# Kernel tuning notes

Hardware: AMD Instinct MI355X
Metric: run time of the kernel (lower is better)

The kernel has to match this reference:

```python
import jax, jax.numpy as jnp
import numpy as np

B, S, UNITS = 64, 2048, 1024


def setup_inputs() -> dict:
    key = jax.random.key(0)
    ks = jax.random.split(key, 6)
    scale = 1.0 / np.sqrt(UNITS)
    return {
        "s_prev": jax.random.normal(ks[0], (B, UNITS), dtype=jnp.float32),
        "hidden_states": jax.random.normal(ks[1], (B, S, UNITS), dtype=jnp.float32),
        "W_w": jax.random.normal(ks[2], (UNITS, UNITS), dtype=jnp.float32) * scale,
        "W_b": jnp.zeros((UNITS,), dtype=jnp.float32),
        "U_w": jax.random.normal(ks[3], (UNITS, UNITS), dtype=jnp.float32) * scale,
        "U_b": jnp.zeros((UNITS,), dtype=jnp.float32),
        "V_w": jax.random.normal(ks[4], (UNITS, 1), dtype=jnp.float32) * scale,
        "V_b": jnp.zeros((1,), dtype=jnp.float32),
    }


def reference(s_prev, hidden_states, W_w, W_b, U_w, U_b, V_w, V_b):
    # W(s_prev): [B, units] -> [B, 1, units]
    W_s = (s_prev @ W_w + W_b)[:, None, :]
    # U(hidden_states): [B, S, units]
    U_h = jnp.einsum('bsu,uk->bsk', hidden_states, U_w) + U_b
    # V(tanh(W_s + U_h)): [B, S, 1]
    scores = jnp.tanh(W_s + U_h) @ V_w + V_b
    # softmax over seq axis
    weights = jax.nn.softmax(scores, axis=1)  # [B, S, 1]
    # weighted sum over seq -> context [B, units]
    context = jnp.sum(weights * hidden_states, axis=1)
    return context, weights
```

## Files before the change

### kernel.cpp

```cpp
#include <hip/hip_runtime.h>

#define BB   64
#define SS   2048
#define UU   1024
#define MM   (BB * SS)

typedef unsigned short u16;
typedef unsigned int   u32;
typedef __attribute__((ext_vector_type(8))) short bf16x8;
typedef __attribute__((ext_vector_type(4))) float f32x4;

__device__ __forceinline__ u16 f2b(float f) {
    u32 x = __float_as_uint(f);
    u32 r = (x + 0x7fffu + ((x >> 16) & 1u)) >> 16;
    return (u16)r;
}
__device__ __forceinline__ float b2f(u16 u) {
    return __uint_as_float(((u32)u) << 16);
}
__device__ __forceinline__ float fast_tanh(float x) {
    x = fminf(fmaxf(x, -15.f), 15.f);
    float e = __expf(2.f * x);
    return (e - 1.f) / (e + 1.f);
}
__device__ __forceinline__ void async_copy16(const u16* gp, u16* lp) {
    __builtin_amdgcn_global_load_lds(
        (const __attribute__((address_space(1))) unsigned int*)gp,
        (__attribute__((address_space(3))) unsigned int*)lp, 16, 0, 0);
}

#define WAITV(N) asm volatile("s_waitcnt vmcnt(" #N ")" ::: "memory")

__global__ __launch_bounds__(256) void k_transpose_uw(const float* __restrict__ Uw,
                                                      u16* __restrict__ UwT) {
    __shared__ float tile[64][65];
    int n0 = blockIdx.x * 64, k0 = blockIdx.y * 64;
    int c = threadIdx.x & 63, r0 = threadIdx.x >> 6;
#pragma unroll
    for (int i = 0; i < 64; i += 4)
        tile[r0 + i][c] = Uw[(size_t)(k0 + r0 + i) * UU + n0 + c];
    __syncthreads();
#pragma unroll
    for (int i = 0; i < 64; i += 4)
        UwT[(size_t)(n0 + r0 + i) * UU + k0 + c] = f2b(tile[c][r0 + i]);
}

__global__ __launch_bounds__(256) void k_convert_h(const float* __restrict__ src,
                                                   u16* __restrict__ dst) {
    size_t i = ((size_t)blockIdx.x * 256 + threadIdx.x) * 8;
    float4 f0 = *(const float4*)(src + i);
    float4 f1 = *(const float4*)(src + i + 4);
    u16 t[8];
    t[0] = f2b(f0.x); t[1] = f2b(f0.y); t[2] = f2b(f0.z); t[3] = f2b(f0.w);
    t[4] = f2b(f1.x); t[5] = f2b(f1.y); t[6] = f2b(f1.z); t[7] = f2b(f1.w);
    *(uint4*)(dst + i) = *(uint4*)t;
}

__global__ __launch_bounds__(256) void k_ws(const float* __restrict__ sp,
                                            const float* __restrict__ Ww,
                                            const float* __restrict__ Wb,
                                            float* __restrict__ Ws) {
    int u = blockIdx.x * 256 + threadIdx.x;
    int b = blockIdx.y;
    int k0 = blockIdx.z * 256;
    const float* sprow = sp + (size_t)b * UU + k0;
    float acc = (blockIdx.z == 0) ? Wb[u] : 0.f;
#pragma unroll 4
    for (int k = 0; k < 256; ++k)
        acc = fmaf(sprow[k], Ww[(size_t)(k0 + k) * UU + u], acc);
    atomicAdd(&Ws[(size_t)b * UU + u], acc);
}

__global__ __launch_bounds__(512, 2) void k_gemm256(const u16* __restrict__ A,
                                                    const u16* __restrict__ UwT,
                                                    const float* __restrict__ Ws,
                                                    const float* __restrict__ Ub,
                                                    const float* __restrict__ Vw,
                                                    float* __restrict__ scp) {
    __shared__ __align__(16) u16 As[4][8192];
    __shared__ __align__(16) u16 Bs[4][8192];
    const int tid  = threadIdx.x;
    const int lane = tid & 63;
    const int wave = tid >> 6;
    const int wm = wave >> 2;
    const int wn = wave & 3;
    const int quad = lane >> 4, l15 = lane & 15;

    const int bid = blockIdx.x;
    const int xcd = bid & 7;
    const int li  = bid >> 3;
    const int mt  = xcd * 64 + (li >> 2);
    const int nt  = li & 3;
    const size_t m0 = (size_t)mt * 256;
    const int n0  = nt * 256;

    const int srow   = lane >> 2;
    const int schunk = (lane & 3) ^ ((srow >> 1) & 3);
    const size_t lane_off = (size_t)srow * UU + (size_t)schunk * 8;
    const int gA = wave * 2;

    int offA[8], offB[4];
#pragma unroll
    for (int mi = 0; mi < 8; ++mi) {
        int r = wm * 128 + mi * 16 + l15;
        offA[mi] = r * 32 + (quad ^ ((r >> 1) & 3)) * 8;
    }
#pragma unroll
    for (int ni = 0; ni < 4; ++ni) {
        int r = wn * 64 + ni * 16 + l15;
        offB[ni] = r * 32 + (quad ^ ((r >> 1) & 3)) * 8;
    }

    f32x4 acc[8][4];
#pragma unroll
    for (int i = 0; i < 8; ++i)
#pragma unroll
        for (int j = 0; j < 4; ++j) acc[i][j] = (f32x4){0.f, 0.f, 0.f, 0.f};

    const u16* Abase = A + m0 * UU;
    const u16* Bbase = UwT + (size_t)n0 * UU;

#define STAGE(kt) do {                                                         \
        const int _b = (kt) & 3;                                               \
        const u16* _ga = Abase + (size_t)(gA * 16) * UU + (kt) * 32 + lane_off;\
        async_copy16(_ga,                  &As[_b][gA * 512]);                 \
        async_copy16(_ga + (size_t)16 * UU, &As[_b][(gA + 1) * 512]);          \
        const u16* _gb = Bbase + (size_t)(gA * 16) * UU + (kt) * 32 + lane_off;\
        async_copy16(_gb,                  &Bs[_b][gA * 512]);                 \
        async_copy16(_gb + (size_t)16 * UU, &Bs[_b][(gA + 1) * 512]);          \
    } while (0)

    auto compute = [&](int kt) {
        const u16* ab = As[kt & 3];
        const u16* bb = Bs[kt & 3];
        bf16x8 a[8], b[4];
#pragma unroll
        for (int mi = 0; mi < 8; ++mi) a[mi] = *(const bf16x8*)(ab + offA[mi]);
#pragma unroll
        for (int ni = 0; ni < 4; ++ni) b[ni] = *(const bf16x8*)(bb + offB[ni]);
        __builtin_amdgcn_s_setprio(1);
#pragma unroll
        for (int mi = 0; mi < 8; ++mi)
#pragma unroll
            for (int ni = 0; ni < 4; ++ni)
                acc[mi][ni] = __builtin_amdgcn_mfma_f32_16x16x32_bf16(
                    a[mi], b[ni], acc[mi][ni], 0, 0, 0);
        __builtin_amdgcn_s_setprio(0);
    };

    STAGE(0); STAGE(1); STAGE(2);

    for (int kt = 0; kt < 29; ++kt) {
        WAITV(8);
        __builtin_amdgcn_sched_barrier(0);
        __builtin_amdgcn_s_barrier();
        STAGE(kt + 3);
        compute(kt);
    }
    WAITV(8); __builtin_amdgcn_sched_barrier(0); __builtin_amdgcn_s_barrier(); compute(29);
    WAITV(4); __builtin_amdgcn_sched_barrier(0); __builtin_amdgcn_s_barrier(); compute(30);
    WAITV(0); __builtin_amdgcn_sched_barrier(0); __builtin_amdgcn_s_barrier(); compute(31);
#undef STAGE

    const int bidx = (int)(m0 >> 11);
    const float* wsrow = Ws + (size_t)bidx * UU;
    float wsv[4], ubv[4], vwv[4];
#pragma unroll
    for (int ni = 0; ni < 4; ++ni) {
        int ng = n0 + wn * 64 + ni * 16 + l15;
        wsv[ni] = wsrow[ng];
        ubv[ni] = Ub[ng];
        vwv[ni] = Vw[ng];
    }
#pragma unroll
    for (int mi = 0; mi < 8; ++mi) {
#pragma unroll
        for (int r = 0; r < 4; ++r) {
            float v = 0.f;
#pragma unroll
            for (int ni = 0; ni < 4; ++ni) {
                float x = acc[mi][ni][r] + wsv[ni] + ubv[ni];
                v = fmaf(fast_tanh(x), vwv[ni], v);
            }
#pragma unroll
            for (int off = 1; off < 16; off <<= 1)
                v += __shfl_xor(v, off, 64);
            if (l15 == 0) {
                size_t mg = m0 + wm * 128 + mi * 16 + quad * 4 + r;
                scp[mg * 16 + nt * 4 + wn] = v;
            }
        }
    }
}

__global__ __launch_bounds__(256) void k_gemm_f32(const float* __restrict__ Aptr,
                                                  const u16* __restrict__ UwT,
                                                  const float* __restrict__ Ws,
                                                  const float* __restrict__ Ub,
                                                  const float* __restrict__ Vw,
                                                  float* __restrict__ scp) {
    __shared__ __align__(16) u16 As[128][72];
    __shared__ __align__(16) u16 Bs[128][72];
    const int tid  = threadIdx.x;
    const int lane = tid & 63;
    const int wave = tid >> 6;
    const int wm = wave >> 1, wn = wave & 1;
    const int quad = lane >> 4, l15 = lane & 15;
    const int nt = blockIdx.x;
    const int n0 = nt * 128;
    const size_t m0 = (size_t)blockIdx.y * 128;

    f32x4 acc[4][4];
#pragma unroll
    for (int i = 0; i < 4; ++i)
#pragma unroll
        for (int j = 0; j < 4; ++j) acc[i][j] = (f32x4){0.f, 0.f, 0.f, 0.f};

    const int sr = tid >> 3;
    const int sc = (tid & 7) * 8;

    for (int kk = 0; kk < UU; kk += 64) {
#pragma unroll
        for (int i = 0; i < 4; ++i) {
            int r = sr + i * 32;
            const float4* p = (const float4*)(Aptr + (m0 + r) * UU + kk + sc);
            float4 f0 = p[0], f1 = p[1];
            u16 t[8];
            t[0] = f2b(f0.x); t[1] = f2b(f0.y); t[2] = f2b(f0.z); t[3] = f2b(f0.w);
            t[4] = f2b(f1.x); t[5] = f2b(f1.y); t[6] = f2b(f1.z); t[7] = f2b(f1.w);
            *(uint4*)(&As[r][sc]) = *(uint4*)t;
        }
#pragma unroll
        for (int i = 0; i < 4; ++i) {
            int r = sr + i * 32;
            uint4 v = *(const uint4*)(UwT + (size_t)(n0 + r) * UU + kk + sc);
            *(uint4*)(&Bs[r][sc]) = v;
        }
        __syncthreads();
#pragma unroll
        for (int k2 = 0; k2 < 64; k2 += 32) {
            bf16x8 a[4], b[4];
#pragma unroll
            for (int mi = 0; mi < 4; ++mi)
                a[mi] = *(const bf16x8*)(&As[wm * 64 + mi * 16 + l15][k2 + quad * 8]);
#pragma unroll
            for (int ni = 0; ni < 4; ++ni)
                b[ni] = *(const bf16x8*)(&Bs[wn * 64 + ni * 16 + l15][k2 + quad * 8]);
#pragma unroll
            for (int mi = 0; mi < 4; ++mi)
#pragma unroll
                for (int ni = 0; ni < 4; ++ni)
                    acc[mi][ni] = __builtin_amdgcn_mfma_f32_16x16x32_bf16(
                        a[mi], b[ni], acc[mi][ni], 0, 0, 0);
        }
        __syncthreads();
    }

    const int bidx = (int)(m0 >> 11);
    const float* wsrow = Ws + (size_t)bidx * UU;
    float wsv[4], ubv[4], vwv[4];
#pragma unroll
    for (int ni = 0; ni < 4; ++ni) {
        int ng = n0 + wn * 64 + ni * 16 + l15;
        wsv[ni] = wsrow[ng];
        ubv[ni] = Ub[ng];
        vwv[ni] = Vw[ng];
    }
#pragma unroll
    for (int mi = 0; mi < 4; ++mi) {
#pragma unroll
        for (int r = 0; r < 4; ++r) {
            float v = 0.f;
#pragma unroll
            for (int ni = 0; ni < 4; ++ni) {
                float x = acc[mi][ni][r] + wsv[ni] + ubv[ni];
                v = fmaf(fast_tanh(x), vwv[ni], v);
            }
#pragma unroll
            for (int off = 1; off < 16; off <<= 1)
                v += __shfl_xor(v, off, 64);
            if (l15 == 0) {
                size_t mg = m0 + wm * 64 + mi * 16 + quad * 4 + r;
                scp[mg * 16 + nt * 2 + wn] = v;
            }
        }
    }
}

__global__ __launch_bounds__(256) void k_softmax(const float* __restrict__ scp,
                                                 float* __restrict__ wout) {
    int b = blockIdx.x, t = threadIdx.x;
    __shared__ float red[256];
    float sc[8];
    float lmax = -1e30f;
#pragma unroll
    for (int i = 0; i < 8; ++i) {
        int s = t + i * 256;
        const float4* p = (const float4*)(scp + ((size_t)b * SS + s) * 16);
        float4 a = p[0], c = p[1], d = p[2], e = p[3];
        float v = (a.x + a.y + a.z + a.w) + (c.x + c.y + c.z + c.w) +
                  (d.x + d.y + d.z + d.w) + (e.x + e.y + e.z + e.w);
        sc[i] = v;
        lmax = fmaxf(lmax, v);
    }
    red[t] = lmax;
    __syncthreads();
    for (int o = 128; o > 0; o >>= 1) {
        if (t < o) red[t] = fmaxf(red[t], red[t + o]);
        __syncthreads();
    }
    float mx = red[0];
    __syncthreads();
    float lsum = 0.f;
#pragma unroll
    for (int i = 0; i < 8; ++i) {
        sc[i] = __expf(sc[i] - mx);
        lsum += sc[i];
    }
    red[t] = lsum;
    __syncthreads();
    for (int o = 128; o > 0; o >>= 1) {
        if (t < o) red[t] += red[t + o];
        __syncthreads();
    }
    float inv = 1.f / red[0];
#pragma unroll
    for (int i = 0; i < 8; ++i)
        wout[(size_t)b * SS + t + i * 256] = sc[i] * inv;
}

template <bool HBF16>
__global__ __launch_bounds__(256) void k_context(const void* __restrict__ hptr,
                                                 const float* __restrict__ w,
                                                 float* __restrict__ ctx) {
    int b = blockIdx.y;
    int s0 = blockIdx.x * 128;
    int u = threadIdx.x * 4;
    const float* wrow = w + (size_t)b * SS + s0;
    float a0 = 0.f, a1 = 0.f, a2 = 0.f, a3 = 0.f;
    for (int i = 0; i < 128; ++i) {
        float wv = wrow[i];
        size_t base = ((size_t)b * SS + s0 + i) * UU + u;
        if (HBF16) {
            ushort4 hv = *(const ushort4*)((const u16*)hptr + base);
            a0 = fmaf(wv, b2f(hv.x), a0);
            a1 = fmaf(wv, b2f(hv.y), a1);
            a2 = fmaf(wv, b2f(hv.z), a2);
            a3 = fmaf(wv, b2f(hv.w), a3);
        } else {
            float4 hv = *(const float4*)((const float*)hptr + base);
            a0 = fmaf(wv, hv.x, a0);
            a1 = fmaf(wv, hv.y, a1);
            a2 = fmaf(wv, hv.z, a2);
            a3 = fmaf(wv, hv.w, a3);
        }
    }
    atomicAdd(&ctx[(size_t)b * UU + u + 0], a0);
    atomicAdd(&ctx[(size_t)b * UU + u + 1], a1);
    atomicAdd(&ctx[(size_t)b * UU + u + 2], a2);
    atomicAdd(&ctx[(size_t)b * UU + u + 3], a3);
}

extern "C" void kernel_launch(void* const* d_in, const int* in_sizes, int n_in,
                              void* d_out, int out_size, void* d_ws, size_t ws_size,
                              hipStream_t stream) {
    const float* s_prev = (const float*)d_in[0];
    const float* h      = (const float*)d_in[1];
    const float* Ww     = (const float*)d_in[2];
    const float* Wb     = (const float*)d_in[3];
    const float* Uw     = (const float*)d_in[4];
    const float* Ub     = (const float*)d_in[5];
    const float* Vw     = (const float*)d_in[6];

    float* out = (float*)d_out;
    char* ws = (char*)d_ws;

    u16*   UwT = (u16*)ws;
    float* Ws  = (float*)(ws + (size_t)(2 << 20));
    float* scp = (float*)(ws + (size_t)(2 << 20) + (256 << 10));
    size_t offH = (size_t)(2 << 20) + (256 << 10) + ((size_t)8 << 20);
    u16*   hbf = (u16*)(ws + offH);
    const size_t hBytes = (size_t)MM * UU * 2;
    const bool useBf16 = (ws_size >= offH + hBytes);

    hipMemsetAsync(out, 0, (size_t)BB * UU * sizeof(float), stream);
    hipMemsetAsync(Ws, 0, (size_t)BB * UU * sizeof(float), stream);

    k_transpose_uw<<<dim3(16, 16), 256, 0, stream>>>(Uw, UwT);
    k_ws<<<dim3(4, BB, 4), 256, 0, stream>>>(s_prev, Ww, Wb, Ws);

    if (useBf16) {
        k_convert_h<<<(MM * (UU / 8)) / 256, 256, 0, stream>>>(h, hbf);
        k_gemm256<<<2048, 512, 0, stream>>>(hbf, UwT, Ws, Ub, Vw, scp);
    } else {
        k_gemm_f32<<<dim3(8, MM / 128), 256, 0, stream>>>(h, UwT, Ws, Ub, Vw, scp);
    }

    k_softmax<<<BB, 256, 0, stream>>>(scp, out + (size_t)BB * UU);

    if (useBf16)
        k_context<true><<<dim3(16, BB), 256, 0, stream>>>(hbf, out + (size_t)BB * UU, out);
    else
        k_context<false><<<dim3(16, BB), 256, 0, stream>>>(h, out + (size_t)BB * UU, out);
}
```

Measured before the change: 1.241 ms.

## Restructure GEMM main loop into ping-pong phases with interleaved staging

```diff
diff --git a/kernel.cpp b/kernel.cpp
--- a/kernel.cpp
+++ b/kernel.cpp
@@ -29,7 +29,9 @@
         (__attribute__((address_space(3))) unsigned int*)lp, 16, 0, 0);
 }
 
-#define WAITV(N) asm volatile("s_waitcnt vmcnt(" #N ")" ::: "memory")
+#define WAITV(N) do { asm volatile("s_waitcnt vmcnt(" #N ")" ::: "memory"); \
+                      __builtin_amdgcn_sched_barrier(0); } while (0)
+#define MF(a_, b_, c_) __builtin_amdgcn_mfma_f32_16x16x32_bf16(a_, b_, c_, 0, 0, 0)
 
 __global__ __launch_bounds__(256) void k_transpose_uw(const float* __restrict__ Uw,
                                                       u16* __restrict__ UwT) {
@@ -77,8 +79,8 @@
                                                     const float* __restrict__ Ub,
                                                     const float* __restrict__ Vw,
                                                     float* __restrict__ scp) {
-    __shared__ __align__(16) u16 As[4][8192];
-    __shared__ __align__(16) u16 Bs[4][8192];
+    __shared__ __align__(16) u16 As[2][2][8192];
+    __shared__ __align__(16) u16 Bs[2][2][8192];
     const int tid  = threadIdx.x;
     const int lane = tid & 63;
     const int wave = tid >> 6;
@@ -96,19 +98,21 @@
 
     const int srow   = lane >> 2;
     const int schunk = (lane & 3) ^ ((srow >> 1) & 3);
-    const size_t lane_off = (size_t)srow * UU + (size_t)schunk * 8;
+    const size_t lane_src = (size_t)srow * UU + (size_t)schunk * 8;
     const int gA = wave * 2;
 
-    int offA[8], offB[4];
-#pragma unroll
-    for (int mi = 0; mi < 8; ++mi) {
-        int r = wm * 128 + mi * 16 + l15;
-        offA[mi] = r * 32 + (quad ^ ((r >> 1) & 3)) * 8;
-    }
+    int offA[2][4], offB[4];
+#pragma unroll
+    for (int mh = 0; mh < 2; ++mh)
+#pragma unroll
+        for (int q = 0; q < 4; ++q) {
+            int r = wm * 128 + mh * 64 + q * 16 + l15;
+            offA[mh][q] = r * 32 + ((quad ^ ((r >> 1) & 3)) << 3);
+        }
 #pragma unroll
     for (int ni = 0; ni < 4; ++ni) {
         int r = wn * 64 + ni * 16 + l15;
-        offB[ni] = r * 32 + (quad ^ ((r >> 1) & 3)) * 8;
+        offB[ni] = r * 32 + ((quad ^ ((r >> 1) & 3)) << 3);
     }
 
     f32x4 acc[8][4];
@@ -120,47 +124,96 @@
     const u16* Abase = A + m0 * UU;
     const u16* Bbase = UwT + (size_t)n0 * UU;
 
-#define STAGE(kt) do {                                                         \
-        const int _b = (kt) & 3;                                               \
-        const u16* _ga = Abase + (size_t)(gA * 16) * UU + (kt) * 32 + lane_off;\
-        async_copy16(_ga,                  &As[_b][gA * 512]);                 \
-        async_copy16(_ga + (size_t)16 * UU, &As[_b][(gA + 1) * 512]);          \
-        const u16* _gb = Bbase + (size_t)(gA * 16) * UU + (kt) * 32 + lane_off;\
-        async_copy16(_gb,                  &Bs[_b][gA * 512]);                 \
-        async_copy16(_gb + (size_t)16 * UU, &Bs[_b][(gA + 1) * 512]);          \
+#define STAGE_A(KT, KH) do {                                                   \
+        const u16* _s = Abase + (size_t)(gA * 16) * UU                         \
+                        + (size_t)((KT) * 64 + (KH) * 32) + lane_src;          \
+        u16* _d = &As[(KT) & 1][KH][gA * 512];                                 \
+        async_copy16(_s, _d);                                                  \
+        async_copy16(_s + (size_t)(16 * UU), _d + 512);                        \
     } while (0)
-
-    auto compute = [&](int kt) {
-        const u16* ab = As[kt & 3];
-        const u16* bb = Bs[kt & 3];
-        bf16x8 a[8], b[4];
-#pragma unroll
-        for (int mi = 0; mi < 8; ++mi) a[mi] = *(const bf16x8*)(ab + offA[mi]);
-#pragma unroll
-        for (int ni = 0; ni < 4; ++ni) b[ni] = *(const bf16x8*)(bb + offB[ni]);
-        __builtin_amdgcn_s_setprio(1);
-#pragma unroll
-        for (int mi = 0; mi < 8; ++mi)
-#pragma unroll
-            for (int ni = 0; ni < 4; ++ni)
-                acc[mi][ni] = __builtin_amdgcn_mfma_f32_16x16x32_bf16(
-                    a[mi], b[ni], acc[mi][ni], 0, 0, 0);
-        __builtin_amdgcn_s_setprio(0);
-    };
-
-    STAGE(0); STAGE(1); STAGE(2);
-
-    for (int kt = 0; kt < 29; ++kt) {
-        WAITV(8);
-        __builtin_amdgcn_sched_barrier(0);
-        __builtin_amdgcn_s_barrier();
-        STAGE(kt + 3);
-        compute(kt);
-    }
-    WAITV(8); __builtin_amdgcn_sched_barrier(0); __builtin_amdgcn_s_barrier(); compute(29);
-    WAITV(4); __builtin_amdgcn_sched_barrier(0); __builtin_amdgcn_s_barrier(); compute(30);
-    WAITV(0); __builtin_amdgcn_sched_barrier(0); __builtin_amdgcn_s_barrier(); compute(31);
-#undef STAGE
+#define STAGE_B(KT, KH) do {                                                   \
+        const u16* _s = Bbase + (size_t)(gA * 16) * UU                         \
+                        + (size_t)((KT) * 64 + (KH) * 32) + lane_src;          \
+        u16* _d = &Bs[(KT) & 1][KH][gA * 512];                                 \
+        async_copy16(_s, _d);                                                  \
+        async_copy16(_s + (size_t)(16 * UU), _d + 512);                        \
+    } while (0)
+
+#define PHASE(MH, KS, STAGE_STMT, TAILGATE_STMT)                               \
+    do {                                                                       \
+        const u16* _ah = &As[buf][KS][0];                                      \
+        if ((MH) == 0) {                                                       \
+            const u16* _bh = &Bs[buf][KS][0];                                  \
+            b[0] = *(const bf16x8*)(_bh + offB[0]);                            \
+            b[1] = *(const bf16x8*)(_bh + offB[1]);                            \
+            b[2] = *(const bf16x8*)(_bh + offB[2]);                            \
+            b[3] = *(const bf16x8*)(_bh + offB[3]);                            \
+        }                                                                      \
+        bf16x8 _a0 = *(const bf16x8*)(_ah + offA[MH][0]);                      \
+        bf16x8 _a1 = *(const bf16x8*)(_ah + offA[MH][1]);                      \
+        bf16x8 _a2 = *(const bf16x8*)(_ah + offA[MH][2]);                      \
+        bf16x8 _a3 = *(const bf16x8*)(_ah + offA[MH][3]);                      \
+        STAGE_STMT;                                                            \
+        asm volatile("s_waitcnt lgkmcnt(0)" ::: "memory");                     \
+        __builtin_amdgcn_sched_barrier(0);                                     \
+        __builtin_amdgcn_s_barrier();                                          \
+        __builtin_amdgcn_sched_barrier(0);                                     \
+        __builtin_amdgcn_s_setprio(1);                                         \
+        acc[(MH)*4+0][0] = MF(_a0, b[0], acc[(MH)*4+0][0]);                    \
+        acc[(MH)*4+0][1] = MF(_a0, b[1], acc[(MH)*4+0][1]);                    \
+        acc[(MH)*4+0][2] = MF(_a0, b[2], acc[(MH)*4+0][2]);                    \
+        acc[(MH)*4+0][3] = MF(_a0, b[3], acc[(MH)*4+0][3]);                    \
+        acc[(MH)*4+1][0] = MF(_a1, b[0], acc[(MH)*4+1][0]);                    \
+        acc[(MH)*4+1][1] = MF(_a1, b[1], acc[(MH)*4+1][1]);                    \
+        acc[(MH)*4+1][2] = MF(_a1, b[2], acc[(MH)*4+1][2]);                    \
+        acc[(MH)*4+1][3] = MF(_a1, b[3], acc[(MH)*4+1][3]);                    \
+        acc[(MH)*4+2][0] = MF(_a2, b[0], acc[(MH)*4+2][0]);                    \
+        acc[(MH)*4+2][1] = MF(_a2, b[1], acc[(MH)*4+2][1]);                    \
+        acc[(MH)*4+2][2] = MF(_a2, b[2], acc[(MH)*4+2][2]);                    \
+        acc[(MH)*4+2][3] = MF(_a2, b[3], acc[(MH)*4+2][3]);                    \
+        acc[(MH)*4+3][0] = MF(_a3, b[0], acc[(MH)*4+3][0]);                    \
+        acc[(MH)*4+3][1] = MF(_a3, b[1], acc[(MH)*4+3][1]);                    \
+        acc[(MH)*4+3][2] = MF(_a3, b[2], acc[(MH)*4+3][2]);                    \
+        acc[(MH)*4+3][3] = MF(_a3, b[3], acc[(MH)*4+3][3]);                    \
+        __builtin_amdgcn_s_setprio(0);                                         \
+        __builtin_amdgcn_sched_barrier(0);                                     \
+        TAILGATE_STMT;                                                         \
+        __builtin_amdgcn_s_barrier();                                          \
+        __builtin_amdgcn_sched_barrier(0);                                     \
+    } while (0)
+
+#define GROUP(G, S0, S1, S2, S3, GATE1, GATE3)                                 \
+    do {                                                                       \
+        const int buf = (G) & 1;                                               \
+        bf16x8 b[4];                                                           \
+        PHASE(0, 0, S0, (void)0);                                              \
+        PHASE(1, 0, S1, GATE1);                                                \
+        PHASE(0, 1, S2, (void)0);                                              \
+        PHASE(1, 1, S3, GATE3);                                                \
+    } while (0)
+
+    STAGE_A(0, 0); STAGE_B(0, 0);
+    STAGE_A(0, 1); STAGE_B(0, 1);
+    STAGE_A(1, 0); STAGE_B(1, 0);
+    WAITV(8);
+    __builtin_amdgcn_s_barrier();
+    __builtin_amdgcn_sched_barrier(0);
+
+#pragma unroll 2
+    for (int g = 0; g < 14; ++g) {
+        GROUP(g, STAGE_A(g + 1, 1), STAGE_B(g + 1, 1),
+                 STAGE_A(g + 2, 0), STAGE_B(g + 2, 0),
+                 WAITV(8), WAITV(8));
+    }
+    GROUP(14, STAGE_A(15, 1), STAGE_B(15, 1), (void)0, (void)0,
+              WAITV(8), WAITV(4));
+    GROUP(15, (void)0, (void)0, (void)0, (void)0,
+              WAITV(0), (void)0);
+
+#undef GROUP
+#undef PHASE
+#undef STAGE_A
+#undef STAGE_B
 
     const int bidx = (int)(m0 >> 11);
     const float* wsrow = Ws + (size_t)bidx * UU;
```

After: 1.191 ms. 4.0% less time.

## Restructure bf16 GEMM main loop into 8-wave ping-pong with BK=64 double buffering

Applied to the files above, without the earlier changes.

```diff
diff --git a/kernel.cpp b/kernel.cpp
--- a/kernel.cpp
+++ b/kernel.cpp
@@ -30,6 +30,10 @@
 }
 
 #define WAITV(N) asm volatile("s_waitcnt vmcnt(" #N ")" ::: "memory")
+#define LGKM0 do { asm volatile("s_waitcnt lgkmcnt(0)" ::: "memory"); \
+                   __builtin_amdgcn_sched_barrier(0); } while (0)
+#define BAR  __builtin_amdgcn_s_barrier()
+#define MF(a_, b_, c_) __builtin_amdgcn_mfma_f32_16x16x32_bf16(a_, b_, c_, 0, 0, 0)
 
 __global__ __launch_bounds__(256) void k_transpose_uw(const float* __restrict__ Uw,
                                                       u16* __restrict__ UwT) {
@@ -77,8 +81,8 @@
                                                     const float* __restrict__ Ub,
                                                     const float* __restrict__ Vw,
                                                     float* __restrict__ scp) {
-    __shared__ __align__(16) u16 As[4][8192];
-    __shared__ __align__(16) u16 Bs[4][8192];
+    __shared__ __align__(16) u16 As[2][16384];
+    __shared__ __align__(16) u16 Bs[2][16384];
     const int tid  = threadIdx.x;
     const int lane = tid & 63;
     const int wave = tid >> 6;
@@ -94,22 +98,18 @@
     const size_t m0 = (size_t)mt * 256;
     const int n0  = nt * 256;
 
-    const int srow   = lane >> 2;
-    const int schunk = (lane & 3) ^ ((srow >> 1) & 3);
-    const size_t lane_off = (size_t)srow * UU + (size_t)schunk * 8;
-    const int gA = wave * 2;
-
-    int offA[8], offB[4];
-#pragma unroll
-    for (int mi = 0; mi < 8; ++mi) {
-        int r = wm * 128 + mi * 16 + l15;
-        offA[mi] = r * 32 + (quad ^ ((r >> 1) & 3)) * 8;
-    }
-#pragma unroll
-    for (int ni = 0; ni < 4; ++ni) {
-        int r = wn * 64 + ni * 16 + l15;
-        offB[ni] = r * 32 + (quad ^ ((r >> 1) & 3)) * 8;
-    }
+    const int srow8  = lane >> 3;
+    const int schunk = (lane & 7) ^ srow8;
+    const size_t lane_src = (size_t)srow8 * UU + (size_t)schunk * 8;
+
+    const int cw = (quad ^ (l15 & 7)) << 3;
+    int offA[4], offB[2];
+#pragma unroll
+    for (int j = 0; j < 4; ++j)
+        offA[j] = (j * 32 + wm * 16 + l15) * 64 + cw;
+#pragma unroll
+    for (int j = 0; j < 2; ++j)
+        offB[j] = (j * 64 + wn * 16 + l15) * 64 + cw;
 
     f32x4 acc[8][4];
 #pragma unroll
@@ -120,54 +120,107 @@
     const u16* Abase = A + m0 * UU;
     const u16* Bbase = UwT + (size_t)n0 * UU;
 
-#define STAGE(kt) do {                                                         \
-        const int _b = (kt) & 3;                                               \
-        const u16* _ga = Abase + (size_t)(gA * 16) * UU + (kt) * 32 + lane_off;\
-        async_copy16(_ga,                  &As[_b][gA * 512]);                 \
-        async_copy16(_ga + (size_t)16 * UU, &As[_b][(gA + 1) * 512]);          \
-        const u16* _gb = Bbase + (size_t)(gA * 16) * UU + (kt) * 32 + lane_off;\
-        async_copy16(_gb,                  &Bs[_b][gA * 512]);                 \
-        async_copy16(_gb + (size_t)16 * UU, &Bs[_b][(gA + 1) * 512]);          \
+    bf16x8 a[4][2], b[4][2];
+
+#define STAGE_A(KT, H) do {                                                    \
+        const u16* _s = Abase + (size_t)((H) * 128 + wave * 16) * UU           \
+                        + (size_t)((KT) * 64) + lane_src;                      \
+        u16* _d = &As[(KT) & 1][((H) * 128 + wave * 16) * 64];                 \
+        async_copy16(_s, _d);                                                  \
+        async_copy16(_s + (size_t)(8 * UU), _d + 512);                         \
     } while (0)
-
-    auto compute = [&](int kt) {
-        const u16* ab = As[kt & 3];
-        const u16* bb = Bs[kt & 3];
-        bf16x8 a[8], b[4];
-#pragma unroll
-        for (int mi = 0; mi < 8; ++mi) a[mi] = *(const bf16x8*)(ab + offA[mi]);
-#pragma unroll
-        for (int ni = 0; ni < 4; ++ni) b[ni] = *(const bf16x8*)(bb + offB[ni]);
-        __builtin_amdgcn_s_setprio(1);
-#pragma unroll
-        for (int mi = 0; mi < 8; ++mi)
-#pragma unroll
-            for (int ni = 0; ni < 4; ++ni)
-                acc[mi][ni] = __builtin_amdgcn_mfma_f32_16x16x32_bf16(
-                    a[mi], b[ni], acc[mi][ni], 0, 0, 0);
-        __builtin_amdgcn_s_setprio(0);
-    };
-
-    STAGE(0); STAGE(1); STAGE(2);
-
-    for (int kt = 0; kt < 29; ++kt) {
-        WAITV(8);
-        __builtin_amdgcn_sched_barrier(0);
-        __builtin_amdgcn_s_barrier();
-        STAGE(kt + 3);
-        compute(kt);
-    }
-    WAITV(8); __builtin_amdgcn_sched_barrier(0); __builtin_amdgcn_s_barrier(); compute(29);
-    WAITV(4); __builtin_amdgcn_sched_barrier(0); __builtin_amdgcn_s_barrier(); compute(30);
-    WAITV(0); __builtin_amdgcn_sched_barrier(0); __builtin_amdgcn_s_barrier(); compute(31);
-#undef STAGE
+#define STAGE_B(KT, H) do {                                                    \
+        const u16* _s = Bbase + (size_t)((H) * 128 + wave * 16) * UU           \
+                        + (size_t)((KT) * 64) + lane_src;                      \
+        u16* _d = &Bs[(KT) & 1][((H) * 128 + wave * 16) * 64];                 \
+        async_copy16(_s, _d);                                                  \
+        async_copy16(_s + (size_t)(8 * UU), _d + 512);                         \
+    } while (0)
+#define READ_A(BUF, MH) do {                                                   \
+        const u16* _p = &As[BUF][(MH) * 8192];                                 \
+        _Pragma("unroll")                                                      \
+        for (int _j = 0; _j < 4; ++_j) {                                       \
+            a[_j][0] = *(const bf16x8*)(_p + offA[_j]);                        \
+            a[_j][1] = *(const bf16x8*)(_p + (offA[_j] ^ 32));                 \
+        }                                                                      \
+    } while (0)
+#define READ_B(BUF, NH) do {                                                   \
+        const u16* _p = &Bs[BUF][(NH) * 8192];                                 \
+        _Pragma("unroll")                                                      \
+        for (int _j = 0; _j < 2; ++_j) {                                       \
+            b[(NH) * 2 + _j][0] = *(const bf16x8*)(_p + offB[_j]);             \
+            b[(NH) * 2 + _j][1] = *(const bf16x8*)(_p + (offB[_j] ^ 32));      \
+        }                                                                      \
+    } while (0)
+#define MMA(MH, NH) do {                                                       \
+        __builtin_amdgcn_s_setprio(1);                                         \
+        _Pragma("unroll")                                                      \
+        for (int _j = 0; _j < 4; ++_j)                                         \
+            _Pragma("unroll")                                                  \
+            for (int _n = 0; _n < 2; ++_n) {                                   \
+                acc[(MH)*4+_j][(NH)*2+_n] =                                    \
+                    MF(a[_j][0], b[(NH)*2+_n][0], acc[(MH)*4+_j][(NH)*2+_n]);  \
+                acc[(MH)*4+_j][(NH)*2+_n] =                                    \
+                    MF(a[_j][1], b[(NH)*2+_n][1], acc[(MH)*4+_j][(NH)*2+_n]);  \
+            }                                                                  \
+        __builtin_amdgcn_s_setprio(0);                                         \
+    } while (0)
+
+    STAGE_A(0, 0); STAGE_A(0, 1); STAGE_B(0, 0); STAGE_B(0, 1);
+    WAITV(2);
+    BAR;
+
+#pragma unroll 2
+    for (int t = 0; t < 15; ++t) {
+        const int buf = t & 1;
+        READ_A(buf, 0); READ_B(buf, 0);
+        STAGE_A(t + 1, 0);
+        BAR; LGKM0;
+        MMA(0, 0);
+        WAITV(2);
+        BAR;
+        READ_B(buf, 1);
+        STAGE_A(t + 1, 1);
+        BAR; LGKM0;
+        MMA(0, 1);
+        BAR;
+        READ_A(buf, 1);
+        STAGE_B(t + 1, 0);
+        BAR; LGKM0;
+        MMA(1, 0);
+        BAR;
+        STAGE_B(t + 1, 1);
+        BAR;
+        MMA(1, 1);
+        WAITV(2);
+        BAR;
+    }
+    READ_A(1, 0); READ_B(1, 0);
+    BAR; LGKM0;
+    MMA(0, 0);
+    WAITV(0);
+    BAR;
+    READ_B(1, 1);
+    BAR; LGKM0;
+    MMA(0, 1);
+    BAR;
+    READ_A(1, 1);
+    BAR; LGKM0;
+    MMA(1, 0);
+    MMA(1, 1);
+
+#undef STAGE_A
+#undef STAGE_B
+#undef READ_A
+#undef READ_B
+#undef MMA
 
     const int bidx = (int)(m0 >> 11);
     const float* wsrow = Ws + (size_t)bidx * UU;
     float wsv[4], ubv[4], vwv[4];
 #pragma unroll
     for (int ni = 0; ni < 4; ++ni) {
-        int ng = n0 + wn * 64 + ni * 16 + l15;
+        int ng = n0 + ni * 64 + wn * 16 + l15;
         wsv[ni] = wsrow[ng];
         ubv[ni] = Ub[ng];
         vwv[ni] = Vw[ng];
@@ -186,7 +239,7 @@
             for (int off = 1; off < 16; off <<= 1)
                 v += __shfl_xor(v, off, 64);
             if (l15 == 0) {
-                size_t mg = m0 + wm * 128 + mi * 16 + quad * 4 + r;
+                size_t mg = m0 + mi * 32 + wm * 16 + quad * 4 + r;
                 scp[mg * 16 + nt * 4 + wn] = v;
             }
         }
```

Result: faster. 1.161 ms (-6.5%).
